# Performance work log

Measured on AMD Instinct MI355X. Metric: run time of the kernel, lower is better.

The kernel has to match this reference:

```python
import jax, jax.numpy as jnp
import numpy as np

NX, NY = 512, 512
DX, DY = 1e-4, 1e-4
VS = 1550.0
DT = 2.5e-8


def setup_inputs() -> dict:
    key = jax.random.key(0)
    k1, k2 = jax.random.split(key)
    sensor_data = jax.random.normal(k1, (4, 2, 128, 2048), dtype=jnp.float32)
    sensor_xy = jax.random.randint(k2, (128, 2), 0, 512, dtype=jnp.int32)
    return {"sensor_data": sensor_data, "sensor_xy": sensor_xy}


def _delay_indices(sensor_xy):
    # pixel grids, 1-indexed as in the torch code (arange(1,513))
    ix = jnp.arange(1, NX + 1, dtype=jnp.float32)[None, :, None]  # (1,Nx,1)
    iy = jnp.arange(1, NY + 1, dtype=jnp.float32)[None, None, :]  # (1,1,Ny)
    x = sensor_xy[:, 0].astype(jnp.float32)[:, None, None]        # (S,1,1)
    y = sensor_xy[:, 1].astype(jnp.float32)[:, None, None]
    dis = jnp.sqrt(((x - ix + 1.0) * DX) ** 2 + ((y - iy + 1.0) * DY) ** 2)  # (S,Nx,Ny)
    # .to(torch.long) truncates; values are non-negative so int cast matches
    return (dis / VS / DT).astype(jnp.int32).reshape(sensor_xy.shape[0], -1)  # (S, Nx*Ny)


def reference(sensor_data, sensor_xy):
    B = sensor_data.shape[0]
    S = sensor_xy.shape[0]
    t = _delay_indices(sensor_xy)                           # (S, P) int32
    data = jnp.transpose(sensor_data, (2, 0, 1, 3))         # (S, B, 2, T)

    def step(img, xs):
        t_s, d_s = xs                                       # (P,), (B,2,T)
        return img + d_s[:, :, t_s], None                   # gather + accumulate

    img0 = jnp.zeros((B, 2, NX * NY), dtype=sensor_data.dtype)
    img, _ = jax.lax.scan(step, img0, (t, data))
    return img.reshape(B, 2, NX, NY)
```

## Files before the change

### kernel.cpp

```cpp
#include <hip/hip_runtime.h>
#include <math.h>


#define NXY 512
#define S_CNT 128
#define T_CNT 2048
#define CH 8
#define CH_STRIDE (S_CNT * T_CNT)
#define NPIX (NXY * NXY)
#define TAB_BYTES (NPIX * 2)

#pragma float_control(push)
#pragma float_control(precise, on)
__device__ __forceinline__ unsigned short delay_entry(int adx, int ady) {
    const double DX32 = (double)1e-4f;
    const double R1 = (double)(float)(1.0 / 1550.0);
    const double R2 = (double)(float)(1.0 / (double)2.5e-8f);
    float dxf = (float)((double)adx * DX32);
    float dyf = (float)((double)ady * DX32);
    float a2 = (float)((double)dxf * (double)dxf);
    float b2 = (float)((double)dyf * (double)dyf);
    float sum = (float)((double)a2 + (double)b2);
    float dis = (float)sqrt((double)sum);
    float q1 = (float)((double)dis * R1);
    float q2 = (float)((double)q1 * R2);
    return (unsigned short)(int)q2;
}

__global__ __launch_bounds__(256) void prep(const float* __restrict__ data,
                                            unsigned short* __restrict__ tab,
                                            float* __restrict__ d2) {
    int idx = blockIdx.x * 256 + threadIdx.x;
    tab[idx] = delay_entry(idx >> 9, idx & 511);

    float v[CH];
#pragma unroll
    for (int k = 0; k < CH; ++k) v[k] = data[k * CH_STRIDE + idx];
    float4* dst = (float4*)(d2 + (size_t)idx * CH);
    dst[0] = make_float4(v[0], v[1], v[2], v[3]);
    dst[1] = make_float4(v[4], v[5], v[6], v[7]);
}
#pragma float_control(pop)

__global__ __launch_bounds__(256) void das_gather8(const float* __restrict__ d2,
                                                   const unsigned short* __restrict__ tab,
                                                   const int* __restrict__ sxy,
                                                   float* __restrict__ out) {
    __shared__ int sx[S_CNT];
    __shared__ int sy[S_CNT];
    int tid = threadIdx.x;
    if (tid < S_CNT) {
        sx[tid] = sxy[2 * tid];
        sy[tid] = sxy[2 * tid + 1];
    }
    __syncthreads();

    int iy = ((blockIdx.x & 31) << 4) | (((tid >> 6) & 1) << 3) | (tid & 7);
    int ix = ((blockIdx.x >> 5) << 4) | ((tid >> 7) << 3) | ((tid >> 3) & 7);

    float4 acc0 = make_float4(0.f, 0.f, 0.f, 0.f);
    float4 acc1 = make_float4(0.f, 0.f, 0.f, 0.f);

#pragma unroll 4
    for (int s = 0; s < S_CNT; ++s) {
        int dxi = sx[s] - ix;
        int dyi = sy[s] - iy;
        int adx = dxi < 0 ? -dxi : dxi;
        int ady = dyi < 0 ? -dyi : dyi;
        int t = (int)tab[(adx << 9) | ady];
        const float4* p = (const float4*)d2 + (((s << 11) + t) << 1);
        float4 v0 = p[0];
        float4 v1 = p[1];
        acc0.x += v0.x;
        acc0.y += v0.y;
        acc0.z += v0.z;
        acc0.w += v0.w;
        acc1.x += v1.x;
        acc1.y += v1.y;
        acc1.z += v1.z;
        acc1.w += v1.w;
    }

    int pix = (ix << 9) | iy;
    out[0 * NPIX + pix] = acc0.x;
    out[1 * NPIX + pix] = acc0.y;
    out[2 * NPIX + pix] = acc0.z;
    out[3 * NPIX + pix] = acc0.w;
    out[4 * NPIX + pix] = acc1.x;
    out[5 * NPIX + pix] = acc1.y;
    out[6 * NPIX + pix] = acc1.z;
    out[7 * NPIX + pix] = acc1.w;
}

#pragma float_control(push)
#pragma float_control(precise, on)
__global__ __launch_bounds__(256) void build_table(unsigned short* __restrict__ tab) {
    int idx = blockIdx.x * 256 + threadIdx.x;
    tab[idx] = delay_entry(idx >> 9, idx & 511);
}
#pragma float_control(pop)

__global__ __launch_bounds__(256) void das_main(const float* __restrict__ data,
                                                const unsigned short* __restrict__ tab,
                                                const int* __restrict__ sxy,
                                                float* __restrict__ out) {
    __shared__ int sx[S_CNT];
    __shared__ int sy[S_CNT];
    int tid = threadIdx.x;
    if (tid < S_CNT) {
        sx[tid] = sxy[2 * tid];
        sy[tid] = sxy[2 * tid + 1];
    }
    __syncthreads();
    int iy = ((blockIdx.x & 31) << 4) | (tid & 15);
    int ix = ((blockIdx.x >> 5) << 4) | (tid >> 4);
    float acc[CH];
#pragma unroll
    for (int k = 0; k < CH; ++k) acc[k] = 0.0f;
#pragma unroll 4
    for (int s = 0; s < S_CNT; ++s) {
        int dxi = sx[s] - ix;
        int dyi = sy[s] - iy;
        int adx = dxi < 0 ? -dxi : dxi;
        int ady = dyi < 0 ? -dyi : dyi;
        int t = (int)tab[(adx << 9) | ady];
        const float* p = data + (s << 11) + t;
#pragma unroll
        for (int k = 0; k < CH; ++k) acc[k] += p[(size_t)k * CH_STRIDE];
    }
    int pix = (ix << 9) | iy;
#pragma unroll
    for (int k = 0; k < CH; ++k) out[k * NPIX + pix] = acc[k];
}

extern "C" void kernel_launch(void* const* d_in, const int* in_sizes, int n_in,
                              void* d_out, int out_size, void* d_ws, size_t ws_size,
                              hipStream_t stream) {
    const float* data = (const float*)d_in[0];
    const int* sxy = (const int*)d_in[1];
    float* out = (float*)d_out;
    unsigned short* tab = (unsigned short*)d_ws;

    size_t need = (size_t)TAB_BYTES + (size_t)CH_STRIDE * CH * sizeof(float);
    if (ws_size >= need) {
        float* d2 = (float*)((char*)d_ws + TAB_BYTES);
        prep<<<NPIX / 256, 256, 0, stream>>>(data, tab, d2);
        das_gather8<<<1024, 256, 0, stream>>>(d2, tab, sxy, out);
    } else {
        build_table<<<NPIX / 256, 256, 0, stream>>>(tab);
        das_main<<<1024, 256, 0, stream>>>(data, tab, sxy, out);
    }
}
```

Before: 119.4 us.

## Split sensor loop across two thread teams with shared-memory reduction

Launches 512-thread blocks where two teams of 256 threads each accumulate half of the 128 sensors for the same pixels, then the second team writes partials to LDS and the first team adds them before storing. This doubles the number of in-flight gather loads per pixel tile to hide memory latency. It costs an extra barrier, 8 KB LDS per block, and changes the floating-point summation order.

```diff
diff --git a/kernel.cpp b/kernel.cpp
--- a/kernel.cpp
+++ b/kernel.cpp
@@ -42,12 +42,13 @@
 }
 #pragma float_control(pop)
 
-__global__ __launch_bounds__(256) void das_gather8(const float* __restrict__ d2,
-                                                   const unsigned short* __restrict__ tab,
-                                                   const int* __restrict__ sxy,
-                                                   float* __restrict__ out) {
+__global__ __launch_bounds__(512) void das_split(const float* __restrict__ d2,
+                                                 const unsigned short* __restrict__ tab,
+                                                 const int* __restrict__ sxy,
+                                                 float* __restrict__ out) {
     __shared__ int sx[S_CNT];
     __shared__ int sy[S_CNT];
+    __shared__ float part[256 * CH];
     int tid = threadIdx.x;
     if (tid < S_CNT) {
         sx[tid] = sxy[2 * tid];
@@ -55,14 +56,18 @@
     }
     __syncthreads();
 
-    int iy = ((blockIdx.x & 31) << 4) | (((tid >> 6) & 1) << 3) | (tid & 7);
-    int ix = ((blockIdx.x >> 5) << 4) | ((tid >> 7) << 3) | ((tid >> 3) & 7);
+    int lid = tid & 255;
+    int team = tid >> 8;
+    int iy = ((blockIdx.x & 31) << 4) | (((lid >> 6) & 1) << 3) | (lid & 7);
+    int ix = ((blockIdx.x >> 5) << 4) | ((lid >> 7) << 3) | ((lid >> 3) & 7);
 
     float4 acc0 = make_float4(0.f, 0.f, 0.f, 0.f);
     float4 acc1 = make_float4(0.f, 0.f, 0.f, 0.f);
 
+    int sbase = team << 6;
 #pragma unroll 4
-    for (int s = 0; s < S_CNT; ++s) {
+    for (int i = 0; i < 64; ++i) {
+        int s = sbase + i;
         int dxi = sx[s] - ix;
         int dyi = sy[s] - iy;
         int adx = dxi < 0 ? -dxi : dxi;
@@ -81,15 +86,26 @@
         acc1.w += v1.w;
     }
 
-    int pix = (ix << 9) | iy;
-    out[0 * NPIX + pix] = acc0.x;
-    out[1 * NPIX + pix] = acc0.y;
-    out[2 * NPIX + pix] = acc0.z;
-    out[3 * NPIX + pix] = acc0.w;
-    out[4 * NPIX + pix] = acc1.x;
-    out[5 * NPIX + pix] = acc1.y;
-    out[6 * NPIX + pix] = acc1.z;
-    out[7 * NPIX + pix] = acc1.w;
+    if (team) {
+        float4* pp = (float4*)(part + lid * CH);
+        pp[0] = acc0;
+        pp[1] = acc1;
+    }
+    __syncthreads();
+    if (!team) {
+        const float4* pp = (const float4*)(part + lid * CH);
+        float4 b0 = pp[0];
+        float4 b1 = pp[1];
+        int pix = (ix << 9) | iy;
+        out[0 * NPIX + pix] = acc0.x + b0.x;
+        out[1 * NPIX + pix] = acc0.y + b0.y;
+        out[2 * NPIX + pix] = acc0.z + b0.z;
+        out[3 * NPIX + pix] = acc0.w + b0.w;
+        out[4 * NPIX + pix] = acc1.x + b1.x;
+        out[5 * NPIX + pix] = acc1.y + b1.y;
+        out[6 * NPIX + pix] = acc1.z + b1.z;
+        out[7 * NPIX + pix] = acc1.w + b1.w;
+    }
 }
 
 #pragma float_control(push)
@@ -145,7 +161,7 @@
     if (ws_size >= need) {
         float* d2 = (float*)((char*)d_ws + TAB_BYTES);
         prep<<<NPIX / 256, 256, 0, stream>>>(data, tab, d2);
-        das_gather8<<<1024, 256, 0, stream>>>(d2, tab, sxy, out);
+        das_split<<<1024, 512, 0, stream>>>(d2, tab, sxy, out);
     } else {
         build_table<<<NPIX / 256, 256, 0, stream>>>(tab);
         das_main<<<1024, 256, 0, stream>>>(data, tab, sxy, out);
```

Result: no change. 120.0 us (+0.5%).
